# Optimization experiments

Hardware: AMD Instinct MI355X
Metric: run time of the kernel (lower is better)

The kernel has to match this reference:

```python
import jax, jax.numpy as jnp
import numpy as np
from jax import lax

V, D, H, K, B, T = 32000, 300, 300, 9, 64, 512


def _lstm_dir(x, w_ih, w_hh, b_ih, b_hh, h0, c0):
    # x: [B, T, D]; torch gate order: i, f, g, o
    def step(carry, xt):
        h, c = carry
        gates = xt @ w_ih.T + h @ w_hh.T + b_ih + b_hh  # [B, 4H]
        i, f, g, o = jnp.split(gates, 4, axis=-1)
        i, f, o = jax.nn.sigmoid(i), jax.nn.sigmoid(f), jax.nn.sigmoid(o)
        g = jnp.tanh(g)
        c = f * c + i * g
        h = o * jnp.tanh(c)
        return (h, c), h

    xs = jnp.transpose(x, (1, 0, 2))  # [T, B, D]
    _, hs = lax.scan(step, (h0, c0), xs)
    return jnp.transpose(hs, (1, 0, 2))  # [B, T, H]


def _emissions(tokens, emb, w_ih_f, w_hh_f, b_ih_f, b_hh_f,
               w_ih_b, w_hh_b, b_ih_b, b_hh_b, h0, c0, w_out, b_out):
    x = emb[tokens]  # [B, T, D]
    hf = _lstm_dir(x, w_ih_f, w_hh_f, b_ih_f, b_hh_f, h0[0], c0[0])
    hb = _lstm_dir(jnp.flip(x, axis=1), w_ih_b, w_hh_b, b_ih_b, b_hh_b, h0[1], c0[1])
    hb = jnp.flip(hb, axis=1)
    out = jnp.concatenate([hf, hb], axis=-1)  # [B, T, 2H]
    return out @ w_out.T + b_out  # [B, T, K]


def _crf_nll(emissions, tags, mask, start_t, end_t, trans):
    # torchcrf: -sum_b log p(tags | emissions)
    e = jnp.transpose(emissions, (1, 0, 2))  # [T, B, K]
    tg = tags.T                               # [T, B]
    m = mask.T.astype(emissions.dtype)        # [T, B]
    bidx = jnp.arange(tags.shape[0])
    # numerator: gold path score
    num = start_t[tg[0]] + e[0][bidx, tg[0]]
    def nstep(carry, inp):
        et, tt, tp, mt = inp
        return carry + (trans[tp, tt] + et[bidx, tt]) * mt, None
    num, _ = lax.scan(nstep, num, (e[1:], tg[1:], tg[:-1], m[1:]))
    last_idx = mask.sum(axis=1).astype(jnp.int32) - 1
    last_tags = tags[bidx, last_idx]
    num = num + end_t[last_tags]
    # denominator: forward algorithm
    alpha = start_t + e[0]  # [B, K]
    def dstep(alpha, inp):
        et, mt = inp
        nxt = jax.scipy.special.logsumexp(alpha[:, :, None] + trans[None], axis=1) + et
        return jnp.where(mt[:, None] > 0, nxt, alpha), None
    alpha, _ = lax.scan(dstep, alpha, (e[1:], m[1:]))
    den = jax.scipy.special.logsumexp(alpha + end_t, axis=1)
    return -jnp.sum(num - den)


def _viterbi(emissions, mask, start_t, end_t, trans):
    e = jnp.transpose(emissions, (1, 0, 2))  # [T, B, K]
    m = mask.T                               # [T, B]
    score = start_t + e[0]                   # [B, K]
    def fstep(score, inp):
        et, mt = inp
        br = score[:, :, None] + trans[None]  # [B, K_prev, K_next]
        best = br.max(axis=1)
        idx = br.argmax(axis=1).astype(jnp.int32)  # [B, K]
        new = best + et
        return jnp.where(mt[:, None], new, score), idx
    score, history = lax.scan(fstep, score, (e[1:], m[1:]))  # history: [T-1, B, K]
    score = score + end_t
    last = jnp.argmax(score, axis=-1).astype(jnp.int32)  # [B]
    def bstep(tag, inp):
        idx_t, mt = inp
        prev = jnp.take_along_axis(idx_t, tag[:, None], axis=1)[:, 0]
        tag = jnp.where(mt, prev, tag)
        return tag, tag
    _, tags_rev = lax.scan(bstep, last, (history, m[1:]), reverse=True)  # [T-1, B]
    path = jnp.concatenate([tags_rev, last[None]], axis=0)  # [T, B]
    return path.T  # [B, T]


def setup_inputs() -> dict:
    key = jax.random.key(0)
    ks = jax.random.split(key, 20)
    s = 0.1
    emb = jax.random.normal(ks[0], (V, D), jnp.float32) * s
    emb = emb.at[0].set(0.0)  # padding_idx row
    inp = {
        "tokens": jax.random.randint(ks[1], (B, T), 0, V, jnp.int32),
        "tags": jax.random.randint(ks[2], (B, T), 0, K, jnp.int32),
        "mask": jnp.ones((B, T), jnp.bool_),
        "emb": emb,
        "w_ih_f": jax.random.normal(ks[3], (4 * H, D), jnp.float32) * s,
        "w_hh_f": jax.random.normal(ks[4], (4 * H, H), jnp.float32) * s,
        "b_ih_f": jax.random.normal(ks[5], (4 * H,), jnp.float32) * s,
        "b_hh_f": jax.random.normal(ks[6], (4 * H,), jnp.float32) * s,
        "w_ih_b": jax.random.normal(ks[7], (4 * H, D), jnp.float32) * s,
        "w_hh_b": jax.random.normal(ks[8], (4 * H, H), jnp.float32) * s,
        "b_ih_b": jax.random.normal(ks[9], (4 * H,), jnp.float32) * s,
        "b_hh_b": jax.random.normal(ks[10], (4 * H,), jnp.float32) * s,
        "h0": jax.random.normal(ks[11], (2, B, H), jnp.float32),
        "c0": jax.random.normal(ks[12], (2, B, H), jnp.float32),
        "w_out": jax.random.normal(ks[13], (K, 2 * H), jnp.float32) * s,
        "b_out": jax.random.normal(ks[14], (K,), jnp.float32) * s,
        "start_t": jax.random.normal(ks[15], (K,), jnp.float32) * s,
        "end_t": jax.random.normal(ks[16], (K,), jnp.float32) * s,
        "trans": jax.random.normal(ks[17], (K, K), jnp.float32) * s,
    }
    return inp


def reference(tokens, tags, mask, emb, w_ih_f, w_hh_f, b_ih_f, b_hh_f,
              w_ih_b, w_hh_b, b_ih_b, b_hh_b, h0, c0, w_out, b_out,
              start_t, end_t, trans):
    feats = _emissions(tokens, emb, w_ih_f, w_hh_f, b_ih_f, b_hh_f,
                       w_ih_b, w_hh_b, b_ih_b, b_hh_b, h0, c0, w_out, b_out)
    paths = _viterbi(feats, mask, start_t, end_t, trans)
    loss = _crf_nll(feats, tags, mask, start_t, end_t, trans)
    return paths, loss
```

## Files before the change

### kernel.cpp

```cpp
#include <hip/hip_runtime.h>
#include <math.h>

#define NV 32000
#define ND 300
#define NH 300
#define NK 9
#define NB 64
#define NT 512

typedef short bf16x8 __attribute__((ext_vector_type(8)));
typedef float f32x4  __attribute__((ext_vector_type(4)));

__device__ inline short bf16r(float x) {
    return (short)((__float_as_uint(x) + 0x8000u) >> 16);
}

#define WB_OFF   0ull
#define WB_F     768000ull
#define E_OFF    (WB_OFF + WB_F)
#define E_SZ     ((unsigned long long)NT*NB*NK)
#define CBUF_OFF (E_OFF + E_SZ)
#define CBUF_SZ  (2ull*NB*NH)
#define HSLOT_OFF (CBUF_OFF + CBUF_SZ)
#define HSLOT_SZ  (2ull*2*NB*NH)
#define XP_OFF   (HSLOT_OFF + HSLOT_SZ)
#define XPC_SZ   (2ull*64*1200*64)

__global__ __launch_bounds__(256) void k_wcvt(
    const float* __restrict__ wihf, const float* __restrict__ wihb,
    const float* __restrict__ whhf, const float* __restrict__ whhb,
    short* __restrict__ dst)
{
    int i = blockIdx.x*256 + threadIdx.x;
    if (i >= 1536000) return;
    int d  = i / 384000;
    int r2 = i % 384000;
    int j  = r2 / 320, k = r2 % 320;
    const float* src = (d == 0) ? wihf : (d == 1) ? wihb : (d == 2) ? whhf : whhb;
    float v = (k < 300) ? src[(size_t)j*300 + k] : 0.f;
    dst[i] = bf16r(v);
}

__global__ __launch_bounds__(256) void k_xproj(
    const int* __restrict__ tokens, const float* __restrict__ emb,
    const short* __restrict__ wb16,
    const float* __restrict__ bif, const float* __restrict__ bhf,
    const float* __restrict__ bib, const float* __restrict__ bhb,
    float* __restrict__ xpc, int chunk)
{
    const int tid = threadIdx.x;
    const int w  = tid >> 6, L = tid & 63;
    const int lm = L & 15, lq = L >> 4;
    const int dir = blockIdx.z;
    const int m0 = blockIdx.x*128 + w*32;
    const int n0 = blockIdx.y*80;
    const int tbase = dir ? (448 - chunk*64) : (chunk*64);

    const float* arow[2];
#pragma unroll
    for (int mi = 0; mi < 2; ++mi) {
        int m = m0 + mi*16 + lm;
        int b = m >> 6, lt = m & 63;
        arow[mi] = emb + (size_t)tokens[b*512 + tbase + lt] * 300;
    }
    const short* brow[5];
#pragma unroll
    for (int ni = 0; ni < 5; ++ni) {
        int j = n0 + ni*16 + lm;
        brow[ni] = wb16 + ((size_t)dir*1200 + j)*320;
    }

    f32x4 acc[2][5];
#pragma unroll
    for (int mi = 0; mi < 2; ++mi)
#pragma unroll
        for (int ni = 0; ni < 5; ++ni)
#pragma unroll
            for (int r = 0; r < 4; ++r) acc[mi][ni][r] = 0.f;

    const float4 z4 = make_float4(0.f,0.f,0.f,0.f);
    for (int k0 = 0; k0 < 320; k0 += 32) {
        const int kk = k0 + lq*8;
        bf16x8 af[2], bf[5];
#pragma unroll
        for (int mi = 0; mi < 2; ++mi) {
            float4 f1 = (kk   < 300) ? *(const float4*)(arow[mi] + kk)     : z4;
            float4 f2 = (kk+4 < 300) ? *(const float4*)(arow[mi] + kk + 4) : z4;
            af[mi][0]=bf16r(f1.x); af[mi][1]=bf16r(f1.y); af[mi][2]=bf16r(f1.z); af[mi][3]=bf16r(f1.w);
            af[mi][4]=bf16r(f2.x); af[mi][5]=bf16r(f2.y); af[mi][6]=bf16r(f2.z); af[mi][7]=bf16r(f2.w);
        }
#pragma unroll
        for (int ni = 0; ni < 5; ++ni)
            bf[ni] = *(const bf16x8*)(brow[ni] + kk);
#pragma unroll
        for (int mi = 0; mi < 2; ++mi)
#pragma unroll
            for (int ni = 0; ni < 5; ++ni)
                acc[mi][ni] = __builtin_amdgcn_mfma_f32_16x16x32_bf16(
                                  af[mi], bf[ni], acc[mi][ni], 0, 0, 0);
    }

#pragma unroll
    for (int ni = 0; ni < 5; ++ni) {
        int j = n0 + ni*16 + lm;
        int g = j/300, rr = j%300;
        int slc = rr/20, ul = rr%20;
        float bias = dir ? (bib[j]+bhb[j]) : (bif[j]+bhf[j]);
#pragma unroll
        for (int mi = 0; mi < 2; ++mi) {
#pragma unroll
            for (int r = 0; r < 4; ++r) {
                int m = m0 + mi*16 + lq*4 + r;
                int b = m >> 6, lt = m & 63;
                int sp = dir ? (63 - lt) : lt;
                size_t idx = ((((size_t)dir*64 + sp)*8 + (b>>3))*15 + slc)*640
                           + (size_t)(b&7)*80 + g*20 + ul;
                xpc[idx] = acc[mi][ni][r] + bias;
            }
        }
    }
}

__global__ __launch_bounds__(256) void k_rnn(
    const float* __restrict__ xpc,
    const short* __restrict__ whh16,
    const float* __restrict__ h0,
    unsigned* hslot, float* __restrict__ cbuf,
    float* __restrict__ ev, const float* __restrict__ wout,
    int s_begin, int s_count, int full)
{
    extern __shared__ char lds_pad[];
    __shared__ __align__(16) short h_sh16[16*328];
    __shared__ __align__(16) float xp_sh[640];
    __shared__ __align__(16) float gates_sh[80*9];
    __shared__ __align__(16) float wo_sh[180];
    __shared__ __align__(16) float hloc[160];
    (void)lds_pad;

    const int tid = threadIdx.x;
    const int wv  = tid >> 6, L = tid & 63;
    const int lm  = L & 15, lq = L >> 4;
    const int dir = blockIdx.x / 120;
    const int rem = blockIdx.x % 120;
    const int sl  = rem / 8;
    const int gb  = rem % 8;
    const int u0  = sl * 20;

    const int tb = (wv == 0) ? 0 : (wv + 1);
    const int tn = (wv == 0) ? 2 : 1;

    bf16x8 A[2][10];
#pragma unroll 2
    for (int mt = 0; mt < 2; ++mt) {
        if (mt < tn) {
            int r = (tb + mt)*16 + lm;
            int grow = (r/20)*300 + u0 + (r%20);
            const short* wr = whh16 + ((size_t)dir*1200 + grow)*320;
#pragma unroll
            for (int ks = 0; ks < 10; ++ks)
                A[mt][ks] = *(const bf16x8*)(wr + ks*32 + lq*8);
        }
    }
    if (tid < 180) wo_sh[tid] = wout[(tid/20)*600 + dir*300 + u0 + (tid%20)];

    for (int i = tid; i < 16*328; i += 256) h_sh16[i] = 0;

    const bool isPW = (tid < 160);
    const int bl_p = tid/20, lu_p = tid%20;
    float c_reg = 0.f;
    if (isPW) c_reg = cbuf[((size_t)dir*NB + gb*8 + bl_p)*NH + u0 + lu_p];

    __syncthreads();

    for (int s = s_begin; s < s_begin + s_count; ++s) {
        const int t = dir ? (511 - s) : s;
        const float* xb; int sp;
        if (full) { xb = xpc + (size_t)(s >> 6)*XPC_SZ; sp = s & 63; }
        else      { xb = xpc;                            sp = s - s_begin; }

        unsigned vb[10];
        unsigned* hsrc = hslot + (((size_t)(s & 1)*2 + dir)*NB + gb*8)*NH;
        if (s > 0 && tid < 240) {
#pragma unroll
            for (int j = 0; j < 10; ++j) {
                int i = tid + 256*j;
                if (i < 2400)
                    vb[j] = __hip_atomic_load(hsrc + i, __ATOMIC_RELAXED,
                                              __HIP_MEMORY_SCOPE_AGENT);
            }
        }

        {
            const float* xsrc = xb + ((((size_t)dir*64 + sp)*8 + gb)*15 + sl)*640;
            if (tid < 160) *(float4*)(&xp_sh[tid*4]) = *(const float4*)(xsrc + tid*4);
        }

        if (s == 0) {
            const float* h0p = h0 + ((size_t)dir*NB + gb*8)*NH;
            for (int i = tid; i < 2400; i += 256)
                h_sh16[(i/300)*328 + (i%300)] = bf16r(h0p[i]);
        } else if (tid < 240) {
            const unsigned tg = (unsigned)s & 0xFFFFu;
            bool ok = false;
            while (!ok) {
                ok = true;
#pragma unroll
                for (int j = 0; j < 10; ++j) {
                    int i = tid + 256*j;
                    if (i < 2400 && (vb[j] >> 16) != tg) {
                        ok = false;
                        vb[j] = __hip_atomic_load(hsrc + i, __ATOMIC_RELAXED,
                                                  __HIP_MEMORY_SCOPE_AGENT);
                    }
                }
            }
#pragma unroll
            for (int j = 0; j < 10; ++j) {
                int i = tid + 256*j;
                if (i < 2400)
                    h_sh16[(i/300)*328 + (i%300)] = (short)(vb[j] & 0xFFFFu);
            }
        }
        __syncthreads();

        {
            bf16x8 Bf[10];
#pragma unroll
            for (int ks = 0; ks < 10; ++ks)
                Bf[ks] = *(const bf16x8*)(h_sh16 + lm*328 + ks*32 + lq*8);
            f32x4 acc[2];
#pragma unroll 2
            for (int mt = 0; mt < 2; ++mt) {
                if (mt < tn) {
#pragma unroll
                    for (int r = 0; r < 4; ++r) acc[mt][r] = 0.f;
#pragma unroll
                    for (int ks = 0; ks < 10; ++ks)
                        acc[mt] = __builtin_amdgcn_mfma_f32_16x16x32_bf16(
                                      A[mt][ks], Bf[ks], acc[mt], 0, 0, 0);
                    if (lm < 8) {
#pragma unroll
                        for (int r = 0; r < 4; ++r)
                            gates_sh[((tb+mt)*16 + lq*4 + r)*9 + lm] = acc[mt][r];
                    }
                }
            }
        }
        __syncthreads();

        if (isPW) {
            float G[4];
#pragma unroll
            for (int g = 0; g < 4; ++g)
                G[g] = xp_sh[bl_p*80 + g*20 + lu_p] + gates_sh[(g*20 + lu_p)*9 + bl_p];
            float ig = 1.f/(1.f+__expf(-G[0]));
            float fg = 1.f/(1.f+__expf(-G[1]));
            float gg = tanhf(G[2]);
            float og = 1.f/(1.f+__expf(-G[3]));
            c_reg = fg*c_reg + ig*gg;
            float h = og*tanhf(c_reg);
            hloc[bl_p*20 + lu_p] = h;
            unsigned hb = (__float_as_uint(h) + 0x8000u) >> 16;
            unsigned pk = (((unsigned)(s+1) & 0xFFFFu) << 16) | hb;
            __hip_atomic_store(
                &hslot[(((size_t)((s+1)&1)*2 + dir)*NB + gb*8 + bl_p)*NH + u0 + lu_p],
                pk, __ATOMIC_RELAXED, __HIP_MEMORY_SCOPE_AGENT);
        }
        __syncthreads();

        if (tid < 72) {
            int b = tid/9, k = tid%9;
            float a = 0.f;
#pragma unroll
            for (int u = 0; u < 20; ++u) a += hloc[b*20+u]*wo_sh[k*20+u];
            atomicAdd(&ev[((size_t)t*NB + gb*8 + b)*NK + k], a);
        }
    }

    if (isPW) cbuf[((size_t)dir*NB + gb*8 + bl_p)*NH + u0 + lu_p] = c_reg;
}

__global__ __launch_bounds__(64) void k_crf(
    const float* __restrict__ ev, const int* __restrict__ tags,
    const float* __restrict__ start_t, const float* __restrict__ end_t,
    const float* __restrict__ trans, const float* __restrict__ bout,
    float* __restrict__ out)
{
    __shared__ __align__(16) float ex_sh[32];
    __shared__ int hist_sh[511*NK];
    const int b = blockIdx.x, ln = threadIdx.x;

    float part = 0.f;
    for (int t = ln; t < NT; t += 64) {
        int tc = tags[b*NT + t];
        float e = ev[((size_t)t*NB + b)*NK + tc] + bout[tc];
        float pre = (t == 0) ? start_t[tc] : trans[tags[b*NT + t - 1]*9 + tc];
        part += pre + e;
    }
    if (ln == 63) part += end_t[tags[b*NT + NT - 1]];
#pragma unroll
    for (int off = 32; off > 0; off >>= 1)
        part += __shfl_down(part, off, 64);
    const float num = part;

    const bool isA = (ln < 9);
    const bool isV = (ln >= 16 && ln < 25);
    const int kc = isV ? (ln - 16) : (isA ? ln : 0);
    float Tc[9];
#pragma unroll
    for (int kp = 0; kp < 9; ++kp) {
        float v = trans[kp*9 + kc];
        Tc[kp] = isA ? __expf(v) : v;
    }
    const float bo = bout[kc];
    float init = start_t[kc] + ev[(size_t)b*NK + kc] + bo;
    if (isA | isV) ex_sh[ln] = init;
    const int base = (ln < 16) ? 0 : 16;

    float etn = ev[((size_t)1*NB + b)*NK + kc] + bo;

    for (int t = 1; t < NT; ++t) {
        float et = etn;
        if (t + 1 < NT) etn = ev[((size_t)(t+1)*NB + b)*NK + kc] + bo;

        float4 s0 = *(const float4*)(&ex_sh[base]);
        float4 s1 = *(const float4*)(&ex_sh[base + 4]);
        float  a8 = ex_sh[base + 8];
        float a0=s0.x,a1=s0.y,a2=s0.z,a3=s0.w,a4=s1.x,a5=s1.y,a6=s1.z,a7=s1.w;

        float outv = 0.f;
        if (isA) {
            float M = fmaxf(fmaxf(fmaxf(a0,a1),fmaxf(a2,a3)),
                            fmaxf(fmaxf(a4,a5),fmaxf(a6,a7)));
            M = fmaxf(M, a8);
            float s =        __expf(a0-M)*Tc[0];
            s = fmaf(__expf(a1-M), Tc[1], s);
            s = fmaf(__expf(a2-M), Tc[2], s);
            s = fmaf(__expf(a3-M), Tc[3], s);
            s = fmaf(__expf(a4-M), Tc[4], s);
            s = fmaf(__expf(a5-M), Tc[5], s);
            s = fmaf(__expf(a6-M), Tc[6], s);
            s = fmaf(__expf(a7-M), Tc[7], s);
            s = fmaf(__expf(a8-M), Tc[8], s);
            outv = M + __logf(s) + et;
        } else if (isV) {
            float bv = a0 + Tc[0]; int arg = 0;
            float v;
            v = a1+Tc[1]; if (v > bv) { bv = v; arg = 1; }
            v = a2+Tc[2]; if (v > bv) { bv = v; arg = 2; }
            v = a3+Tc[3]; if (v > bv) { bv = v; arg = 3; }
            v = a4+Tc[4]; if (v > bv) { bv = v; arg = 4; }
            v = a5+Tc[5]; if (v > bv) { bv = v; arg = 5; }
            v = a6+Tc[6]; if (v > bv) { bv = v; arg = 6; }
            v = a7+Tc[7]; if (v > bv) { bv = v; arg = 7; }
            v = a8+Tc[8]; if (v > bv) { bv = v; arg = 8; }
            outv = bv + et;
            hist_sh[(t-1)*NK + (ln-16)] = arg;
        }
        if (isA | isV) ex_sh[ln] = outv;
    }

    if (ln == 0) {
        float M = -1e30f;
#pragma unroll
        for (int k = 0; k < 9; ++k) M = fmaxf(M, ex_sh[k] + end_t[k]);
        float ls = 0.f;
#pragma unroll
        for (int k = 0; k < 9; ++k) ls += __expf(ex_sh[k] + end_t[k] - M);
        float den = M + __logf(ls);
        atomicAdd(out + NB*NT, den - num);

        float best = -1e30f; int last = 0;
#pragma unroll
        for (int k = 0; k < 9; ++k) {
            float v = ex_sh[16 + k] + end_t[k];
            if (v > best) { best = v; last = k; }
        }
        int* pout = (int*)out;
        pout[b*NT + NT - 1] = last;
        for (int i = NT - 2; i >= 0; --i) {
            last = hist_sh[i*NK + last];
            pout[b*NT + i] = last;
        }
    }
}

extern "C" void kernel_launch(void* const* d_in, const int* in_sizes, int n_in,
                              void* d_out, int out_size, void* d_ws, size_t ws_size,
                              hipStream_t stream)
{
    (void)in_sizes; (void)n_in;

    const int*   tokens = (const int*)  d_in[0];
    const int*   tags   = (const int*)  d_in[1];
    const float* emb    = (const float*)d_in[3];
    const float* wihf   = (const float*)d_in[4];
    const float* whhf   = (const float*)d_in[5];
    const float* bihf   = (const float*)d_in[6];
    const float* bhhf   = (const float*)d_in[7];
    const float* wihb   = (const float*)d_in[8];
    const float* whhb   = (const float*)d_in[9];
    const float* bib    = (const float*)d_in[10];
    const float* bhhb   = (const float*)d_in[11];
    const float* h0     = (const float*)d_in[12];
    const float* c0     = (const float*)d_in[13];
    const float* wout   = (const float*)d_in[14];
    const float* bout   = (const float*)d_in[15];
    const float* startt = (const float*)d_in[16];
    const float* endt   = (const float*)d_in[17];
    const float* trans  = (const float*)d_in[18];

    float* ws    = (float*)d_ws;
    short* wb16  = (short*)(ws + WB_OFF);
    short* whh16 = wb16 + 768000;
    float* evp   = ws + E_OFF;
    float* cbuf  = ws + CBUF_OFF;
    unsigned* hslot = (unsigned*)(ws + HSLOT_OFF);
    float* xp    = ws + XP_OFF;
    float* out   = (float*)d_out;

    const size_t need_full = (XP_OFF + 8ull*XPC_SZ) * 4ull;
    const bool full = (ws_size >= need_full);

    (void)hipMemsetAsync(d_out, 0, (size_t)out_size * sizeof(float), stream);
    (void)hipMemsetAsync(evp, 0, (size_t)E_SZ * sizeof(float), stream);
    (void)hipMemcpyAsync(cbuf, c0, 2ull*NB*NH*sizeof(float), hipMemcpyDeviceToDevice, stream);

    k_wcvt<<<6000, 256, 0, stream>>>(wihf, wihb, whhf, whhb, wb16);

    if (full) {
        for (int c = 0; c < 8; ++c)
            k_xproj<<<dim3(32, 15, 2), 256, 0, stream>>>(
                tokens, emb, wb16, bihf, bhhf, bib, bhhb, xp + (size_t)c*XPC_SZ, c);
        k_rnn<<<240, 256, 81920, stream>>>(
            xp, whh16, h0, hslot, cbuf, evp, wout, 0, 512, 1);
    } else {
        for (int c = 0; c < 8; ++c) {
            k_xproj<<<dim3(32, 15, 2), 256, 0, stream>>>(
                tokens, emb, wb16, bihf, bhhf, bib, bhhb, xp, c);
            k_rnn<<<240, 256, 81920, stream>>>(
                xp, whh16, h0, hslot, cbuf, evp, wout, c*64, 64, 0);
        }
    }
    k_crf<<<64, 64, 0, stream>>>(evp, tags, startt, endt, trans, bout, out);
}
```

Baseline: 1.967 ms.

## Split CRF forward/Viterbi into separate waves, parallelize backtrace, use fast tanh

The CRF kernel now runs the forward algorithm and the Viterbi recursion in two separate wavefronts. Each wave exchanges state through shuffles instead of shared memory. The serial Viterbi backtrace becomes chunked: first it composes per-chunk state maps in parallel, then it chains the chunk entry points, then it decodes the chunks in parallel. Separately, the LSTM cell replaces tanhf with an exp-based approximation and moves the local h store after the atomic slot publish, trading a little accuracy for fewer instructions on the recurrent critical path.

After: 1.913 ms. 2.8% less time.

```diff
diff --git a/kernel.cpp b/kernel.cpp
--- a/kernel.cpp
+++ b/kernel.cpp
@@ -13,6 +13,11 @@
 
 __device__ inline short bf16r(float x) {
     return (short)((__float_as_uint(x) + 0x8000u) >> 16);
+}
+
+__device__ inline float tanh_fast(float x) {
+    float e2 = __expf(2.f * x);
+    return 1.f - 2.f / (e2 + 1.f);
 }
 
 #define WB_OFF   0ull
@@ -255,16 +260,16 @@
                 G[g] = xp_sh[bl_p*80 + g*20 + lu_p] + gates_sh[(g*20 + lu_p)*9 + bl_p];
             float ig = 1.f/(1.f+__expf(-G[0]));
             float fg = 1.f/(1.f+__expf(-G[1]));
-            float gg = tanhf(G[2]);
+            float gg = tanh_fast(G[2]);
             float og = 1.f/(1.f+__expf(-G[3]));
             c_reg = fg*c_reg + ig*gg;
-            float h = og*tanhf(c_reg);
-            hloc[bl_p*20 + lu_p] = h;
+            float h = og*tanh_fast(c_reg);
             unsigned hb = (__float_as_uint(h) + 0x8000u) >> 16;
             unsigned pk = (((unsigned)(s+1) & 0xFFFFu) << 16) | hb;
             __hip_atomic_store(
                 &hslot[(((size_t)((s+1)&1)*2 + dir)*NB + gb*8 + bl_p)*NH + u0 + lu_p],
                 pk, __ATOMIC_RELAXED, __HIP_MEMORY_SCOPE_AGENT);
+            hloc[bl_p*20 + lu_p] = h;
         }
         __syncthreads();
 
@@ -280,109 +285,157 @@
     if (isPW) cbuf[((size_t)dir*NB + gb*8 + bl_p)*NH + u0 + lu_p] = c_reg;
 }
 
-__global__ __launch_bounds__(64) void k_crf(
+#define BT_C 14
+#define BT_L 37
+
+__global__ __launch_bounds__(128) void k_crf(
     const float* __restrict__ ev, const int* __restrict__ tags,
     const float* __restrict__ start_t, const float* __restrict__ end_t,
     const float* __restrict__ trans, const float* __restrict__ bout,
     float* __restrict__ out)
 {
-    __shared__ __align__(16) float ex_sh[32];
     __shared__ int hist_sh[511*NK];
-    const int b = blockIdx.x, ln = threadIdx.x;
-
-    float part = 0.f;
-    for (int t = ln; t < NT; t += 64) {
-        int tc = tags[b*NT + t];
-        float e = ev[((size_t)t*NB + b)*NK + tc] + bout[tc];
-        float pre = (t == 0) ? start_t[tc] : trans[tags[b*NT + t - 1]*9 + tc];
-        part += pre + e;
-    }
-    if (ln == 63) part += end_t[tags[b*NT + NT - 1]];
-#pragma unroll
-    for (int off = 32; off > 0; off >>= 1)
-        part += __shfl_down(part, off, 64);
-    const float num = part;
-
-    const bool isA = (ln < 9);
-    const bool isV = (ln >= 16 && ln < 25);
-    const int kc = isV ? (ln - 16) : (isA ? ln : 0);
-    float Tc[9];
-#pragma unroll
-    for (int kp = 0; kp < 9; ++kp) {
-        float v = trans[kp*9 + kc];
-        Tc[kp] = isA ? __expf(v) : v;
-    }
-    const float bo = bout[kc];
-    float init = start_t[kc] + ev[(size_t)b*NK + kc] + bo;
-    if (isA | isV) ex_sh[ln] = init;
-    const int base = (ln < 16) ? 0 : 16;
-
-    float etn = ev[((size_t)1*NB + b)*NK + kc] + bo;
-
-    for (int t = 1; t < NT; ++t) {
-        float et = etn;
-        if (t + 1 < NT) etn = ev[((size_t)(t+1)*NB + b)*NK + kc] + bo;
-
-        float4 s0 = *(const float4*)(&ex_sh[base]);
-        float4 s1 = *(const float4*)(&ex_sh[base + 4]);
-        float  a8 = ex_sh[base + 8];
-        float a0=s0.x,a1=s0.y,a2=s0.z,a3=s0.w,a4=s1.x,a5=s1.y,a6=s1.z,a7=s1.w;
-
-        float outv = 0.f;
-        if (isA) {
-            float M = fmaxf(fmaxf(fmaxf(a0,a1),fmaxf(a2,a3)),
-                            fmaxf(fmaxf(a4,a5),fmaxf(a6,a7)));
-            M = fmaxf(M, a8);
-            float s =        __expf(a0-M)*Tc[0];
-            s = fmaf(__expf(a1-M), Tc[1], s);
-            s = fmaf(__expf(a2-M), Tc[2], s);
-            s = fmaf(__expf(a3-M), Tc[3], s);
-            s = fmaf(__expf(a4-M), Tc[4], s);
-            s = fmaf(__expf(a5-M), Tc[5], s);
-            s = fmaf(__expf(a6-M), Tc[6], s);
-            s = fmaf(__expf(a7-M), Tc[7], s);
-            s = fmaf(__expf(a8-M), Tc[8], s);
-            outv = M + __logf(s) + et;
-        } else if (isV) {
-            float bv = a0 + Tc[0]; int arg = 0;
-            float v;
-            v = a1+Tc[1]; if (v > bv) { bv = v; arg = 1; }
-            v = a2+Tc[2]; if (v > bv) { bv = v; arg = 2; }
-            v = a3+Tc[3]; if (v > bv) { bv = v; arg = 3; }
-            v = a4+Tc[4]; if (v > bv) { bv = v; arg = 4; }
-            v = a5+Tc[5]; if (v > bv) { bv = v; arg = 5; }
-            v = a6+Tc[6]; if (v > bv) { bv = v; arg = 6; }
-            v = a7+Tc[7]; if (v > bv) { bv = v; arg = 7; }
-            v = a8+Tc[8]; if (v > bv) { bv = v; arg = 8; }
-            outv = bv + et;
-            hist_sh[(t-1)*NK + (ln-16)] = arg;
-        }
-        if (isA | isV) ex_sh[ln] = outv;
-    }
-
-    if (ln == 0) {
-        float M = -1e30f;
-#pragma unroll
-        for (int k = 0; k < 9; ++k) M = fmaxf(M, ex_sh[k] + end_t[k]);
-        float ls = 0.f;
-#pragma unroll
-        for (int k = 0; k < 9; ++k) ls += __expf(ex_sh[k] + end_t[k] - M);
-        float den = M + __logf(ls);
-        atomicAdd(out + NB*NT, den - num);
-
-        float best = -1e30f; int last = 0;
-#pragma unroll
-        for (int k = 0; k < 9; ++k) {
-            float v = ex_sh[16 + k] + end_t[k];
-            if (v > best) { best = v; last = k; }
-        }
-        int* pout = (int*)out;
-        pout[b*NT + NT - 1] = last;
-        for (int i = NT - 2; i >= 0; --i) {
-            last = hist_sh[i*NK + last];
-            pout[b*NT + i] = last;
-        }
-    }
+    __shared__ int fmap[BT_C*NK];
+    __shared__ int entry_sh[BT_C];
+    __shared__ int last_sh;
+
+    const int b   = blockIdx.x;
+    const int tid = threadIdx.x;
+    const int wv  = tid >> 6;
+    const int ln  = tid & 63;
+    const int kc  = (ln < 9) ? ln : 8;
+
+    if (wv == 0) {
+        float part = 0.f;
+        for (int t = ln; t < NT; t += 64) {
+            int tc = tags[b*NT + t];
+            float e = ev[((size_t)t*NB + b)*NK + tc] + bout[tc];
+            float pre = (t == 0) ? start_t[tc] : trans[tags[b*NT + t - 1]*9 + tc];
+            part += pre + e;
+        }
+        if (ln == 63) part += end_t[tags[b*NT + NT - 1]];
+#pragma unroll
+        for (int off = 32; off > 0; off >>= 1)
+            part += __shfl_down(part, off, 64);
+        const float num = part;
+
+        float Tc[9];
+#pragma unroll
+        for (int kp = 0; kp < 9; ++kp) Tc[kp] = __expf(trans[kp*9 + kc]);
+        const float bo = bout[kc];
+        float a = start_t[kc] + ev[(size_t)b*NK + kc] + bo;
+        float et1 = ev[((size_t)1*NB + b)*NK + kc] + bo;
+        float et2 = ev[((size_t)2*NB + b)*NK + kc] + bo;
+
+        for (int t = 1; t < NT; ++t) {
+            float et = et1; et1 = et2;
+            if (t + 2 < NT) et2 = ev[((size_t)(t+2)*NB + b)*NK + kc] + bo;
+
+            float s0=__shfl(a,0), s1=__shfl(a,1), s2=__shfl(a,2),
+                  s3=__shfl(a,3), s4=__shfl(a,4), s5=__shfl(a,5),
+                  s6=__shfl(a,6), s7=__shfl(a,7), s8=__shfl(a,8);
+            float M = fmaxf(fmaxf(fmaxf(s0,s1),fmaxf(s2,s3)),
+                            fmaxf(fmaxf(s4,s5),fmaxf(fmaxf(s6,s7),s8)));
+            float p0=__expf(s0-M)*Tc[0], p1=__expf(s1-M)*Tc[1],
+                  p2=__expf(s2-M)*Tc[2], p3=__expf(s3-M)*Tc[3],
+                  p4=__expf(s4-M)*Tc[4], p5=__expf(s5-M)*Tc[5],
+                  p6=__expf(s6-M)*Tc[6], p7=__expf(s7-M)*Tc[7],
+                  p8=__expf(s8-M)*Tc[8];
+            float s = ((p0+p1)+(p2+p3)) + ((p4+p5)+(p6+p7)) + p8;
+            a = M + __logf(s) + et;
+        }
+
+        float af = a + end_t[kc];
+        float f0=__shfl(af,0), f1=__shfl(af,1), f2=__shfl(af,2),
+              f3=__shfl(af,3), f4=__shfl(af,4), f5=__shfl(af,5),
+              f6=__shfl(af,6), f7=__shfl(af,7), f8=__shfl(af,8);
+        if (ln == 0) {
+            float M = fmaxf(fmaxf(fmaxf(f0,f1),fmaxf(f2,f3)),
+                            fmaxf(fmaxf(f4,f5),fmaxf(fmaxf(f6,f7),f8)));
+            float ls = __expf(f0-M)+__expf(f1-M)+__expf(f2-M)+__expf(f3-M)
+                     + __expf(f4-M)+__expf(f5-M)+__expf(f6-M)+__expf(f7-M)
+                     + __expf(f8-M);
+            float den = M + __logf(ls);
+            atomicAdd(out + NB*NT, den - num);
+        }
+    } else {
+        float Tc[9];
+#pragma unroll
+        for (int kp = 0; kp < 9; ++kp) Tc[kp] = trans[kp*9 + kc];
+        const float bo = bout[kc];
+        float v = start_t[kc] + ev[(size_t)b*NK + kc] + bo;
+        float et1 = ev[((size_t)1*NB + b)*NK + kc] + bo;
+        float et2 = ev[((size_t)2*NB + b)*NK + kc] + bo;
+
+        for (int t = 1; t < NT; ++t) {
+            float et = et1; et1 = et2;
+            if (t + 2 < NT) et2 = ev[((size_t)(t+2)*NB + b)*NK + kc] + bo;
+
+            float s0=__shfl(v,0), s1=__shfl(v,1), s2=__shfl(v,2),
+                  s3=__shfl(v,3), s4=__shfl(v,4), s5=__shfl(v,5),
+                  s6=__shfl(v,6), s7=__shfl(v,7), s8=__shfl(v,8);
+            float bv = s0 + Tc[0]; int arg = 0;
+            float x;
+            x = s1+Tc[1]; if (x > bv) { bv = x; arg = 1; }
+            x = s2+Tc[2]; if (x > bv) { bv = x; arg = 2; }
+            x = s3+Tc[3]; if (x > bv) { bv = x; arg = 3; }
+            x = s4+Tc[4]; if (x > bv) { bv = x; arg = 4; }
+            x = s5+Tc[5]; if (x > bv) { bv = x; arg = 5; }
+            x = s6+Tc[6]; if (x > bv) { bv = x; arg = 6; }
+            x = s7+Tc[7]; if (x > bv) { bv = x; arg = 7; }
+            x = s8+Tc[8]; if (x > bv) { bv = x; arg = 8; }
+            if (ln < 9) hist_sh[(t-1)*NK + ln] = arg;
+            v = bv + et;
+        }
+
+        float vf = v + end_t[kc];
+        float f0=__shfl(vf,0), f1=__shfl(vf,1), f2=__shfl(vf,2),
+              f3=__shfl(vf,3), f4=__shfl(vf,4), f5=__shfl(vf,5),
+              f6=__shfl(vf,6), f7=__shfl(vf,7), f8=__shfl(vf,8);
+        if (ln == 0) {
+            float best = f0; int last = 0;
+            if (f1 > best) { best = f1; last = 1; }
+            if (f2 > best) { best = f2; last = 2; }
+            if (f3 > best) { best = f3; last = 3; }
+            if (f4 > best) { best = f4; last = 4; }
+            if (f5 > best) { best = f5; last = 5; }
+            if (f6 > best) { best = f6; last = 6; }
+            if (f7 > best) { best = f7; last = 7; }
+            if (f8 > best) { best = f8; last = 8; }
+            last_sh = last;
+        }
+    }
+
+    __syncthreads();
+
+    if (tid < BT_C*NK) {
+        int c = tid / NK, s = tid % NK;
+        int lo = c*BT_L, hi = min(511, lo + BT_L);
+        int pos = s;
+        for (int i = hi - 1; i >= lo; --i) pos = hist_sh[i*NK + pos];
+        fmap[c*NK + s] = pos;
+    }
+    __syncthreads();
+    if (tid == 0) {
+        int e = last_sh;
+        entry_sh[BT_C-1] = e;
+        for (int c = BT_C - 2; c >= 0; --c) {
+            e = fmap[(c+1)*NK + e];
+            entry_sh[c] = e;
+        }
+    }
+    __syncthreads();
+    int* pout = (int*)out;
+    if (tid < BT_C) {
+        int c = tid;
+        int lo = c*BT_L, hi = min(511, lo + BT_L);
+        int pos = entry_sh[c];
+        for (int i = hi - 1; i >= lo; --i) {
+            pos = hist_sh[i*NK + pos];
+            pout[b*NT + i] = pos;
+        }
+    }
+    if (tid == 0) pout[b*NT + NT - 1] = last_sh;
 }
 
 extern "C" void kernel_launch(void* const* d_in, const int* in_sizes, int n_in,
@@ -442,5 +495,5 @@
                 xp, whh16, h0, hslot, cbuf, evp, wout, c*64, 64, 0);
         }
     }
-    k_crf<<<64, 64, 0, stream>>>(evp, tags, startt, endt, trans, bout, out);
-}
+    k_crf<<<64, 128, 0, stream>>>(evp, tags, startt, endt, trans, bout, out);
+}
```
